# Kernel tuning notes

Hardware: AMD Instinct MI355X
Metric: run time of the kernel (lower is better)

## Reference

```python
import jax, jax.numpy as jnp
import numpy as np

N = 50000      # nodes
E = 800000     # edges (avg degree 16)
DIN = 128
HID = 128
OUT = 10       # classes
G = 64         # graphs in batch


def setup_inputs() -> dict:
    key = jax.random.key(0)
    ks = jax.random.split(key, 10)
    x = jax.random.normal(ks[0], (N, DIN), dtype=jnp.float32)
    edge_index = jax.random.randint(ks[1], (2, E), 0, N, dtype=jnp.int32)
    edge_weight = jax.random.uniform(ks[2], (E,), dtype=jnp.float32)
    batch = jnp.sort(jax.random.randint(ks[3], (N,), 0, G, dtype=jnp.int32))
    W1 = jax.random.normal(ks[4], (DIN, HID), dtype=jnp.float32) / np.sqrt(DIN)
    b1 = jnp.zeros((HID,), dtype=jnp.float32)
    W2 = jax.random.normal(ks[5], (HID, HID), dtype=jnp.float32) / np.sqrt(HID)
    b2 = jnp.zeros((HID,), dtype=jnp.float32)
    W3 = jax.random.normal(ks[6], (HID, OUT), dtype=jnp.float32) / np.sqrt(HID)
    b3 = jnp.zeros((OUT,), dtype=jnp.float32)
    return {"x": x, "edge_index": edge_index, "edge_weight": edge_weight,
            "batch": batch, "W1": W1, "b1": b1, "W2": W2, "b2": b2,
            "W3": W3, "b3": b3}


def _gcn_norm(edge_index, edge_weight, n_nodes):
    # PyG gcn_norm: add self-loops with weight 1, D^-1/2 (A+I) D^-1/2
    loop = jnp.arange(n_nodes, dtype=edge_index.dtype)
    src = jnp.concatenate([edge_index[0], loop])
    dst = jnp.concatenate([edge_index[1], loop])
    w = jnp.concatenate([edge_weight, jnp.ones((n_nodes,), edge_weight.dtype)])
    deg = jax.ops.segment_sum(w, dst, num_segments=n_nodes)
    dinv = jnp.where(deg > 0, jax.lax.rsqrt(deg), 0.0)
    norm = dinv[src] * w * dinv[dst]
    return src, dst, norm


def _gcn_conv(x, W, b, src, dst, norm, n_nodes):
    h = x @ W                                      # [N, F] dense transform
    msg = norm[:, None] * h[src]                   # gather + scale  [E+N, F]
    out = jax.ops.segment_sum(msg, dst, num_segments=n_nodes)  # scatter-add
    return out + b


def reference(x, edge_index, edge_weight, batch, W1, b1, W2, b2, W3, b3):
    src, dst, norm = _gcn_norm(edge_index, edge_weight, N)
    h = jax.nn.relu(_gcn_conv(x, W1, b1, src, dst, norm, N))
    h = jax.nn.relu(_gcn_conv(h, W2, b2, src, dst, norm, N))
    h = _gcn_conv(h, W3, b3, src, dst, norm, N)    # [N, OUT]
    # global_mean_pool over graph ids
    sums = jax.ops.segment_sum(h, batch, num_segments=G)          # [G, OUT]
    cnts = jax.ops.segment_sum(jnp.ones((N,), h.dtype), batch, num_segments=G)
    pooled = sums / jnp.maximum(cnts, 1.0)[:, None]
    return jax.nn.log_softmax(pooled, axis=1)
```

## Files before the change

### kernel.cpp

```cpp
#include <hip/hip_runtime.h>
#include <math.h>

#define NN 50000
#define EE 800000
#define GG 64
#define FD 128
#define OUTD 10
#define NB 49

typedef __attribute__((ext_vector_type(8))) short s8v;
typedef __attribute__((ext_vector_type(4))) float f4v;

static __device__ inline unsigned short f2b(float f) {
    unsigned int u = __float_as_uint(f);
    return (unsigned short)((u + 0x7FFFu + ((u >> 16) & 1u)) >> 16);
}

#define DEG_SCALE 4294967296.0
#define DEG_MASK  ((1ull << 44) - 1)


__global__ void k_init(unsigned long long* packed, int n) {
    int i = blockIdx.x * blockDim.x + threadIdx.x;
    if (i < n) packed[i] = (1ull << 44) | (1ull << 32);
}

__global__ void k_degree(const int* __restrict__ dst, const float* __restrict__ w,
                         unsigned long long* packed, unsigned* __restrict__ rank, int e) {
    int i = blockIdx.x * blockDim.x + threadIdx.x;
    if (i >= e) return;
    unsigned long long q = (unsigned long long)((double)w[i] * DEG_SCALE + 0.5);
    unsigned long long old = atomicAdd(&packed[dst[i]], (1ull << 44) | q);
    rank[i] = (unsigned)(old >> 44) - 1u;
}

__global__ void k_dinv(const unsigned long long* __restrict__ packed,
                       int* __restrict__ cnt, float* __restrict__ dinv, int n) {
    int i = blockIdx.x * blockDim.x + threadIdx.x;
    if (i >= n) return;
    unsigned long long p = packed[i];
    cnt[i] = (int)(p >> 44);
    float deg = (float)((double)(p & DEG_MASK) * (1.0 / DEG_SCALE));
    dinv[i] = 1.0f / sqrtf(deg);
}

__global__ __launch_bounds__(1024) void k_scanA(const int* __restrict__ cnt,
        int* __restrict__ rowptr, int* __restrict__ blocksum, int n) {
    __shared__ int wtot[16];
    int tid = threadIdx.x;
    int i = blockIdx.x * 1024 + tid;
    int lane = tid & 63, wv = tid >> 6;
    int v = (i < n) ? cnt[i] : 0;
    int s = v;
    #pragma unroll
    for (int off = 1; off < 64; off <<= 1) {
        int u = __shfl_up(s, off, 64);
        if (lane >= off) s += u;
    }
    if (lane == 63) wtot[wv] = s;
    __syncthreads();
    int wpre = 0;
    for (int j = 0; j < wv; ++j) wpre += wtot[j];
    if (i < n) rowptr[i] = wpre + s - v;
    if (tid == 1023) blocksum[blockIdx.x] = wpre + s;
}

__global__ void k_scanB(int* blocksum, int* rowptr) {
    int l = threadIdx.x;
    int v = (l < NB) ? blocksum[l] : 0;
    int s = v;
    #pragma unroll
    for (int off = 1; off < 64; off <<= 1) {
        int u = __shfl_up(s, off, 64);
        if (l >= off) s += u;
    }
    if (l < NB) blocksum[l] = s - v;
    if (l == NB - 1) rowptr[NN] = s;
}

__global__ __launch_bounds__(1024) void k_scanC(int* __restrict__ rowptr,
        const int* __restrict__ blocksum, int n) {
    int i = blockIdx.x * 1024 + threadIdx.x;
    if (i >= n) return;
    rowptr[i] += blocksum[blockIdx.x];
}

__global__ void k_fill(const int* __restrict__ src, const int* __restrict__ dst,
                       const float* __restrict__ w, const float* __restrict__ dinv,
                       const int* __restrict__ rowptr, const unsigned* __restrict__ rank,
                       uint2* __restrict__ ent, int e) {
    int i = blockIdx.x * blockDim.x + threadIdx.x;
    if (i >= e) return;
    int s = src[i], d = dst[i];
    int pos = rowptr[d] + (int)rank[i];
    float v = dinv[s] * w[i] * dinv[d];
    ent[pos] = make_uint2((unsigned)s, __float_as_uint(v));
}

__global__ void k_selfloop(const int* __restrict__ rowptr, const float* __restrict__ dinv,
                           uint2* __restrict__ ent, int n) {
    int i = blockIdx.x * blockDim.x + threadIdx.x;
    if (i >= n) return;
    float di = dinv[i];
    ent[rowptr[i + 1] - 1] = make_uint2((unsigned)i, __float_as_uint(di * di));
}

__global__ void k_bounds(const int* __restrict__ batch, int* __restrict__ gstart, int n) {
    int i = blockIdx.x * blockDim.x + threadIdx.x;
    if (i >= n) return;
    int b = batch[i];
    int bp = (i == 0) ? -1 : batch[i - 1];
    for (int g = bp + 1; g <= b; ++g) gstart[g] = i;
    if (i == n - 1)
        for (int g = b + 1; g <= GG; ++g) gstart[g] = n;
}


__global__ void k_cvt(const float* __restrict__ in, unsigned short* __restrict__ out, int n8) {
    int i = blockIdx.x * blockDim.x + threadIdx.x;
    if (i >= n8) return;
    const float4* p = (const float4*)in + (size_t)i * 2;
    float4 a = p[0], b = p[1];
    uint4 r;
    r.x = (unsigned)f2b(a.x) | ((unsigned)f2b(a.y) << 16);
    r.y = (unsigned)f2b(a.z) | ((unsigned)f2b(a.w) << 16);
    r.z = (unsigned)f2b(b.x) | ((unsigned)f2b(b.y) << 16);
    r.w = (unsigned)f2b(b.z) | ((unsigned)f2b(b.w) << 16);
    *((uint4*)out + i) = r;
}

__global__ void k_w128t(const float* __restrict__ W, unsigned short* __restrict__ Wt) {
    int i = blockIdx.x * blockDim.x + threadIdx.x;
    if (i >= FD * FD) return;
    int nn = i >> 7, k = i & 127;
    Wt[i] = f2b(W[k * FD + nn]);
}

__global__ __launch_bounds__(256) void k_gemm_bf(const unsigned short* __restrict__ A,
        const unsigned short* __restrict__ Wt, unsigned short* __restrict__ out, int n) {
    int tid = threadIdx.x;
    int wave = tid >> 6, lane = tid & 63;
    int quad = lane >> 4, c16 = lane & 15;
    int rowbase = blockIdx.x * 64 + wave * 16;
    int rowA = rowbase + c16;
    if (rowA >= n) rowA = n - 1;
    f4v acc[8];
    #pragma unroll
    for (int t = 0; t < 8; ++t) acc[t] = (f4v){0.f, 0.f, 0.f, 0.f};

    #pragma unroll
    for (int k0 = 0; k0 < 128; k0 += 32) {
        s8v a = *(const s8v*)(A + (size_t)rowA * FD + k0 + quad * 8);
        #pragma unroll
        for (int t = 0; t < 8; ++t) {
            s8v b = *(const s8v*)(Wt + (size_t)(t * 16 + c16) * FD + k0 + quad * 8);
            acc[t] = __builtin_amdgcn_mfma_f32_16x16x32_bf16(a, b, acc[t], 0, 0, 0);
        }
    }
    #pragma unroll
    for (int t = 0; t < 8; ++t) {
        #pragma unroll
        for (int r = 0; r < 4; ++r) {
            int row = rowbase + quad * 4 + r;
            if (row < n) out[(size_t)row * FD + t * 16 + c16] = f2b(acc[t][r]);
        }
    }
}

__global__ void k_gemm10(const unsigned short* __restrict__ A, const float* __restrict__ W,
                         float* __restrict__ out, int n) {
    __shared__ float Ws[FD * OUTD];
    int tid = threadIdx.x;
    for (int i = tid; i < FD * OUTD; i += blockDim.x) Ws[i] = W[i];
    __syncthreads();
    int i = blockIdx.x * blockDim.x + tid;
    if (i >= n) return;
    float acc[OUTD];
    #pragma unroll
    for (int c = 0; c < OUTD; ++c) acc[c] = 0.0f;
    const unsigned short* a = A + (size_t)i * FD;
    for (int k0 = 0; k0 < FD; k0 += 8) {
        uint4 t = *(const uint4*)(a + k0);
        float av[8];
        av[0] = __uint_as_float(t.x << 16); av[1] = __uint_as_float(t.x & 0xFFFF0000u);
        av[2] = __uint_as_float(t.y << 16); av[3] = __uint_as_float(t.y & 0xFFFF0000u);
        av[4] = __uint_as_float(t.z << 16); av[5] = __uint_as_float(t.z & 0xFFFF0000u);
        av[6] = __uint_as_float(t.w << 16); av[7] = __uint_as_float(t.w & 0xFFFF0000u);
        #pragma unroll
        for (int j = 0; j < 8; ++j)
            #pragma unroll
            for (int c = 0; c < OUTD; ++c) acc[c] += av[j] * Ws[(k0 + j) * OUTD + c];
    }
    float* o = out + (size_t)i * OUTD;
    #pragma unroll
    for (int c = 0; c < OUTD; ++c) o[c] = acc[c];
}

__global__ __launch_bounds__(256) void k_spmm_bf(const int* __restrict__ rowptr,
        const uint2* __restrict__ ent, const unsigned short* __restrict__ tin,
        const float* __restrict__ bias, unsigned short* __restrict__ out,
        int n, int dorelu) {
    int w = (blockIdx.x * blockDim.x + threadIdx.x) >> 6;
    int lane = threadIdx.x & 63;
    if (w >= n) return;
    int c = lane & 15, g = lane >> 4;
    int beg = rowptr[w], end = rowptr[w + 1];
    float acc[8];
    #pragma unroll
    for (int j = 0; j < 8; ++j) acc[j] = 0.0f;
    for (int e0 = beg; e0 < end; e0 += 8) {
        int e1 = e0 + g, e2 = e0 + 4 + g;
        uint2 en1 = (e1 < end) ? ent[e1] : make_uint2(0u, 0u);
        uint2 en2 = (e2 < end) ? ent[e2] : make_uint2(0u, 0u);
        uint4 t1 = *(const uint4*)(tin + (size_t)en1.x * FD + c * 8);
        uint4 t2 = *(const uint4*)(tin + (size_t)en2.x * FD + c * 8);
        float v1 = __uint_as_float(en1.y), v2 = __uint_as_float(en2.y);
        acc[0] += v1 * __uint_as_float(t1.x << 16);
        acc[1] += v1 * __uint_as_float(t1.x & 0xFFFF0000u);
        acc[2] += v1 * __uint_as_float(t1.y << 16);
        acc[3] += v1 * __uint_as_float(t1.y & 0xFFFF0000u);
        acc[4] += v1 * __uint_as_float(t1.z << 16);
        acc[5] += v1 * __uint_as_float(t1.z & 0xFFFF0000u);
        acc[6] += v1 * __uint_as_float(t1.w << 16);
        acc[7] += v1 * __uint_as_float(t1.w & 0xFFFF0000u);
        acc[0] += v2 * __uint_as_float(t2.x << 16);
        acc[1] += v2 * __uint_as_float(t2.x & 0xFFFF0000u);
        acc[2] += v2 * __uint_as_float(t2.y << 16);
        acc[3] += v2 * __uint_as_float(t2.y & 0xFFFF0000u);
        acc[4] += v2 * __uint_as_float(t2.z << 16);
        acc[5] += v2 * __uint_as_float(t2.z & 0xFFFF0000u);
        acc[6] += v2 * __uint_as_float(t2.w << 16);
        acc[7] += v2 * __uint_as_float(t2.w & 0xFFFF0000u);
    }
    #pragma unroll
    for (int j = 0; j < 8; ++j) {
        acc[j] += __shfl_xor(acc[j], 16, 64);
        acc[j] += __shfl_xor(acc[j], 32, 64);
    }
    if (g == 0) {
        uint4 r;
        float o[8];
        #pragma unroll
        for (int j = 0; j < 8; ++j) {
            float x = acc[j] + bias[c * 8 + j];
            o[j] = dorelu ? fmaxf(x, 0.0f) : x;
        }
        r.x = (unsigned)f2b(o[0]) | ((unsigned)f2b(o[1]) << 16);
        r.y = (unsigned)f2b(o[2]) | ((unsigned)f2b(o[3]) << 16);
        r.z = (unsigned)f2b(o[4]) | ((unsigned)f2b(o[5]) << 16);
        r.w = (unsigned)f2b(o[6]) | ((unsigned)f2b(o[7]) << 16);
        *(uint4*)(out + (size_t)w * FD + c * 8) = r;
    }
}

__global__ void k_spmm10(const int* __restrict__ rowptr, const uint2* __restrict__ ent,
        const float* __restrict__ tin, const float* __restrict__ bias,
        float* __restrict__ out, int n) {
    int t = blockIdx.x * blockDim.x + threadIdx.x;
    int node = t / OUTD;
    int c = t - node * OUTD;
    if (node >= n) return;
    int beg = rowptr[node], end = rowptr[node + 1];
    float acc = 0.0f;
    for (int e = beg; e < end; ++e) {
        uint2 en = ent[e];
        acc += __uint_as_float(en.y) * tin[(size_t)en.x * OUTD + c];
    }
    out[(size_t)node * OUTD + c] = acc + bias[c];
}


__global__ __launch_bounds__(256) void k_poolfin(const float* __restrict__ h,
        const int* __restrict__ gstart, float* __restrict__ out) {
    int g = blockIdx.x;
    int beg = gstart[g], end = gstart[g + 1];
    int tid = threadIdx.x;
    int lane = tid & 63, wv = tid >> 6;
    float acc[OUTD];
    #pragma unroll
    for (int c = 0; c < OUTD; ++c) acc[c] = 0.0f;
    for (int i = beg + tid; i < end; i += 256) {
        const float* hp = h + (size_t)i * OUTD;
        #pragma unroll
        for (int c = 0; c < OUTD; ++c) acc[c] += hp[c];
    }
    #pragma unroll
    for (int off = 32; off >= 1; off >>= 1)
        #pragma unroll
        for (int c = 0; c < OUTD; ++c) acc[c] += __shfl_down(acc[c], off, 64);
    __shared__ float ws[4][OUTD];
    if (lane == 0)
        #pragma unroll
        for (int c = 0; c < OUTD; ++c) ws[wv][c] = acc[c];
    __syncthreads();
    if (tid == 0) {
        float cf = fmaxf((float)(end - beg), 1.0f);
        float v[OUTD], m = -1e30f;
        #pragma unroll
        for (int c = 0; c < OUTD; ++c) {
            v[c] = (ws[0][c] + ws[1][c] + ws[2][c] + ws[3][c]) / cf;
            m = fmaxf(m, v[c]);
        }
        float s = 0.0f;
        #pragma unroll
        for (int c = 0; c < OUTD; ++c) s += expf(v[c] - m);
        float l = logf(s);
        #pragma unroll
        for (int c = 0; c < OUTD; ++c) out[g * OUTD + c] = v[c] - m - l;
    }
}


extern "C" void kernel_launch(void* const* d_in, const int* in_sizes, int n_in,
                              void* d_out, int out_size, void* d_ws, size_t ws_size,
                              hipStream_t stream) {
    const float* x   = (const float*)d_in[0];
    const int*   ei  = (const int*)d_in[1];
    const float* ew  = (const float*)d_in[2];
    const int*   bat = (const int*)d_in[3];
    const float* W1  = (const float*)d_in[4];
    const float* b1  = (const float*)d_in[5];
    const float* W2  = (const float*)d_in[6];
    const float* b2  = (const float*)d_in[7];
    const float* W3  = (const float*)d_in[8];
    const float* b3  = (const float*)d_in[9];
    float* out = (float*)d_out;

    const int* src = ei;
    const int* dst = ei + EE;

    char* p = (char*)d_ws;
    auto alloc = [&](size_t bytes) -> void* {
        void* r = (void*)p;
        p += (bytes + 255) & ~(size_t)255;
        return r;
    };
    unsigned long long* packed = (unsigned long long*)alloc((size_t)NN * 8);
    int*            cnt    = (int*)  alloc((size_t)NN * 4);
    float*          dinv   = (float*)alloc((size_t)NN * 4);
    int*            rowptr = (int*)  alloc((size_t)(NN + 1) * 4);
    unsigned*       rank   = (unsigned*)alloc((size_t)EE * 4);
    uint2*          ent    = (uint2*)alloc((size_t)(EE + NN) * 8);
    unsigned short* xbf    = (unsigned short*)alloc((size_t)NN * FD * 2);
    unsigned short* Wt1    = (unsigned short*)alloc((size_t)FD * FD * 2);
    unsigned short* Wt2    = (unsigned short*)alloc((size_t)FD * FD * 2);
    unsigned short* hA     = (unsigned short*)alloc((size_t)NN * FD * 2);
    unsigned short* hB     = (unsigned short*)alloc((size_t)NN * FD * 2);
    float*          bufC   = (float*)alloc((size_t)NN * OUTD * 4);
    float*          bufD   = (float*)alloc((size_t)NN * OUTD * 4);
    int*            bsum   = (int*)  alloc((size_t)(NB + 1) * 4);
    int*            gstart = (int*)  alloc((size_t)(GG + 1) * 4);
    (void)ws_size; (void)in_sizes; (void)n_in; (void)out_size;

    const int B = 256;
    k_init    <<<(NN + B - 1) / B, B, 0, stream>>>(packed, NN);
    k_degree  <<<(EE + B - 1) / B, B, 0, stream>>>(dst, ew, packed, rank, EE);
    k_dinv    <<<(NN + B - 1) / B, B, 0, stream>>>(packed, cnt, dinv, NN);
    k_scanA   <<<NB, 1024, 0, stream>>>(cnt, rowptr, bsum, NN);
    k_scanB   <<<1, 64, 0, stream>>>(bsum, rowptr);
    k_scanC   <<<NB, 1024, 0, stream>>>(rowptr, bsum, NN);
    k_fill    <<<(EE + B - 1) / B, B, 0, stream>>>(src, dst, ew, dinv, rowptr, rank, ent, EE);
    k_selfloop<<<(NN + B - 1) / B, B, 0, stream>>>(rowptr, dinv, ent, NN);
    k_bounds  <<<(NN + B - 1) / B, B, 0, stream>>>(bat, gstart, NN);
    k_cvt     <<<(NN * FD / 8 + B - 1) / B, B, 0, stream>>>(x, xbf, NN * FD / 8);
    k_w128t   <<<(FD * FD + B - 1) / B, B, 0, stream>>>(W1, Wt1);
    k_w128t   <<<(FD * FD + B - 1) / B, B, 0, stream>>>(W2, Wt2);

    k_gemm_bf<<<(NN + 63) / 64, B, 0, stream>>>(xbf, Wt1, hA, NN);
    k_spmm_bf<<<(NN * 64 + B - 1) / B, B, 0, stream>>>(rowptr, ent, hA, b1, hB, NN, 1);
    k_gemm_bf<<<(NN + 63) / 64, B, 0, stream>>>(hB, Wt2, hA, NN);
    k_spmm_bf<<<(NN * 64 + B - 1) / B, B, 0, stream>>>(rowptr, ent, hA, b2, hB, NN, 1);
    k_gemm10 <<<(NN + B - 1) / B, B, 0, stream>>>(hB, W3, bufC, NN);
    k_spmm10 <<<(NN * OUTD + B - 1) / B, B, 0, stream>>>(rowptr, ent, bufC, b3, bufD, NN);
    k_poolfin<<<GG, 256, 0, stream>>>(bufD, gstart, out);
}
```

Before: 309.2 us.

## Fuse preprocessing kernels, convert input in GEMM, deepen SpMM edge unrolling

Merges the weight transposes into the init kernel, the dinv computation into the first scan pass, and the self-loop insertion into the final scan pass, cutting several kernel launches and intermediate buffers. The first GEMM now reads fp32 x directly and rounds it to bf16 in registers, so the separate conversion pass and its extra round trip through memory go away. The SpMM inner loop now handles 16 edges per iteration with four independent gathers in flight, raising memory-level parallelism at the cost of more registers.

```diff
diff --git a/kernel.cpp b/kernel.cpp
--- a/kernel.cpp
+++ b/kernel.cpp
@@ -20,9 +20,16 @@
 #define DEG_MASK  ((1ull << 44) - 1)
 
 
-__global__ void k_init(unsigned long long* packed, int n) {
+__global__ void k_prep(unsigned long long* packed, const float* __restrict__ W1,
+                       const float* __restrict__ W2, unsigned short* __restrict__ Wt1,
+                       unsigned short* __restrict__ Wt2, int n) {
     int i = blockIdx.x * blockDim.x + threadIdx.x;
     if (i < n) packed[i] = (1ull << 44) | (1ull << 32);
+    if (i < FD * FD) {
+        int nn = i >> 7, k = i & 127;
+        Wt1[i] = f2b(W1[k * FD + nn]);
+        Wt2[i] = f2b(W2[k * FD + nn]);
+    }
 }
 
 __global__ void k_degree(const int* __restrict__ dst, const float* __restrict__ w,
@@ -34,23 +41,20 @@
     rank[i] = (unsigned)(old >> 44) - 1u;
 }
 
-__global__ void k_dinv(const unsigned long long* __restrict__ packed,
-                       int* __restrict__ cnt, float* __restrict__ dinv, int n) {
-    int i = blockIdx.x * blockDim.x + threadIdx.x;
-    if (i >= n) return;
-    unsigned long long p = packed[i];
-    cnt[i] = (int)(p >> 44);
-    float deg = (float)((double)(p & DEG_MASK) * (1.0 / DEG_SCALE));
-    dinv[i] = 1.0f / sqrtf(deg);
-}
-
-__global__ __launch_bounds__(1024) void k_scanA(const int* __restrict__ cnt,
-        int* __restrict__ rowptr, int* __restrict__ blocksum, int n) {
+__global__ __launch_bounds__(1024) void k_scanA(const unsigned long long* __restrict__ packed,
+        int* __restrict__ rowptr, int* __restrict__ blocksum,
+        float* __restrict__ dinv, int n) {
     __shared__ int wtot[16];
     int tid = threadIdx.x;
     int i = blockIdx.x * 1024 + tid;
     int lane = tid & 63, wv = tid >> 6;
-    int v = (i < n) ? cnt[i] : 0;
+    int v = 0;
+    if (i < n) {
+        unsigned long long p = packed[i];
+        v = (int)(p >> 44);
+        float deg = (float)((double)(p & DEG_MASK) * (1.0 / DEG_SCALE));
+        dinv[i] = 1.0f / sqrtf(deg);
+    }
     int s = v;
     #pragma unroll
     for (int off = 1; off < 64; off <<= 1) {
@@ -79,10 +83,15 @@
 }
 
 __global__ __launch_bounds__(1024) void k_scanC(int* __restrict__ rowptr,
-        const int* __restrict__ blocksum, int n) {
+        const int* __restrict__ blocksum, const unsigned long long* __restrict__ packed,
+        const float* __restrict__ dinv, uint2* __restrict__ ent, int n) {
     int i = blockIdx.x * 1024 + threadIdx.x;
     if (i >= n) return;
-    rowptr[i] += blocksum[blockIdx.x];
+    int r = rowptr[i] + blocksum[blockIdx.x];
+    rowptr[i] = r;
+    int cnt = (int)(packed[i] >> 44);
+    float di = dinv[i];
+    ent[r + cnt - 1] = make_uint2((unsigned)i, __float_as_uint(di * di));
 }
 
 __global__ void k_fill(const int* __restrict__ src, const int* __restrict__ dst,
@@ -97,14 +106,6 @@
     ent[pos] = make_uint2((unsigned)s, __float_as_uint(v));
 }
 
-__global__ void k_selfloop(const int* __restrict__ rowptr, const float* __restrict__ dinv,
-                           uint2* __restrict__ ent, int n) {
-    int i = blockIdx.x * blockDim.x + threadIdx.x;
-    if (i >= n) return;
-    float di = dinv[i];
-    ent[rowptr[i + 1] - 1] = make_uint2((unsigned)i, __float_as_uint(di * di));
-}
-
 __global__ void k_bounds(const int* __restrict__ batch, int* __restrict__ gstart, int n) {
     int i = blockIdx.x * blockDim.x + threadIdx.x;
     if (i >= n) return;
@@ -115,25 +116,42 @@
         for (int g = b + 1; g <= GG; ++g) gstart[g] = n;
 }
 
-
-__global__ void k_cvt(const float* __restrict__ in, unsigned short* __restrict__ out, int n8) {
-    int i = blockIdx.x * blockDim.x + threadIdx.x;
-    if (i >= n8) return;
-    const float4* p = (const float4*)in + (size_t)i * 2;
-    float4 a = p[0], b = p[1];
-    uint4 r;
-    r.x = (unsigned)f2b(a.x) | ((unsigned)f2b(a.y) << 16);
-    r.y = (unsigned)f2b(a.z) | ((unsigned)f2b(a.w) << 16);
-    r.z = (unsigned)f2b(b.x) | ((unsigned)f2b(b.y) << 16);
-    r.w = (unsigned)f2b(b.z) | ((unsigned)f2b(b.w) << 16);
-    *((uint4*)out + i) = r;
-}
-
-__global__ void k_w128t(const float* __restrict__ W, unsigned short* __restrict__ Wt) {
-    int i = blockIdx.x * blockDim.x + threadIdx.x;
-    if (i >= FD * FD) return;
-    int nn = i >> 7, k = i & 127;
-    Wt[i] = f2b(W[k * FD + nn]);
+__global__ __launch_bounds__(256) void k_gemm_f32in(const float* __restrict__ A,
+        const unsigned short* __restrict__ Wt, unsigned short* __restrict__ out, int n) {
+    int tid = threadIdx.x;
+    int wave = tid >> 6, lane = tid & 63;
+    int quad = lane >> 4, c16 = lane & 15;
+    int rowbase = blockIdx.x * 64 + wave * 16;
+    int rowA = rowbase + c16;
+    if (rowA >= n) rowA = n - 1;
+    f4v acc[8];
+    #pragma unroll
+    for (int t = 0; t < 8; ++t) acc[t] = (f4v){0.f, 0.f, 0.f, 0.f};
+
+    #pragma unroll
+    for (int k0 = 0; k0 < 128; k0 += 32) {
+        const float* ap = A + (size_t)rowA * FD + k0 + quad * 8;
+        float4 a0 = *(const float4*)ap;
+        float4 a1 = *(const float4*)(ap + 4);
+        s8v a;
+        a[0] = (short)f2b(a0.x); a[1] = (short)f2b(a0.y);
+        a[2] = (short)f2b(a0.z); a[3] = (short)f2b(a0.w);
+        a[4] = (short)f2b(a1.x); a[5] = (short)f2b(a1.y);
+        a[6] = (short)f2b(a1.z); a[7] = (short)f2b(a1.w);
+        #pragma unroll
+        for (int t = 0; t < 8; ++t) {
+            s8v b = *(const s8v*)(Wt + (size_t)(t * 16 + c16) * FD + k0 + quad * 8);
+            acc[t] = __builtin_amdgcn_mfma_f32_16x16x32_bf16(a, b, acc[t], 0, 0, 0);
+        }
+    }
+    #pragma unroll
+    for (int t = 0; t < 8; ++t) {
+        #pragma unroll
+        for (int r = 0; r < 4; ++r) {
+            int row = rowbase + quad * 4 + r;
+            if (row < n) out[(size_t)row * FD + t * 16 + c16] = f2b(acc[t][r]);
+        }
+    }
 }
 
 __global__ __launch_bounds__(256) void k_gemm_bf(const unsigned short* __restrict__ A,
@@ -208,29 +226,29 @@
     float acc[8];
     #pragma unroll
     for (int j = 0; j < 8; ++j) acc[j] = 0.0f;
-    for (int e0 = beg; e0 < end; e0 += 8) {
-        int e1 = e0 + g, e2 = e0 + 4 + g;
-        uint2 en1 = (e1 < end) ? ent[e1] : make_uint2(0u, 0u);
-        uint2 en2 = (e2 < end) ? ent[e2] : make_uint2(0u, 0u);
-        uint4 t1 = *(const uint4*)(tin + (size_t)en1.x * FD + c * 8);
-        uint4 t2 = *(const uint4*)(tin + (size_t)en2.x * FD + c * 8);
-        float v1 = __uint_as_float(en1.y), v2 = __uint_as_float(en2.y);
-        acc[0] += v1 * __uint_as_float(t1.x << 16);
-        acc[1] += v1 * __uint_as_float(t1.x & 0xFFFF0000u);
-        acc[2] += v1 * __uint_as_float(t1.y << 16);
-        acc[3] += v1 * __uint_as_float(t1.y & 0xFFFF0000u);
-        acc[4] += v1 * __uint_as_float(t1.z << 16);
-        acc[5] += v1 * __uint_as_float(t1.z & 0xFFFF0000u);
-        acc[6] += v1 * __uint_as_float(t1.w << 16);
-        acc[7] += v1 * __uint_as_float(t1.w & 0xFFFF0000u);
-        acc[0] += v2 * __uint_as_float(t2.x << 16);
-        acc[1] += v2 * __uint_as_float(t2.x & 0xFFFF0000u);
-        acc[2] += v2 * __uint_as_float(t2.y << 16);
-        acc[3] += v2 * __uint_as_float(t2.y & 0xFFFF0000u);
-        acc[4] += v2 * __uint_as_float(t2.z << 16);
-        acc[5] += v2 * __uint_as_float(t2.z & 0xFFFF0000u);
-        acc[6] += v2 * __uint_as_float(t2.w << 16);
-        acc[7] += v2 * __uint_as_float(t2.w & 0xFFFF0000u);
+    for (int e0 = beg; e0 < end; e0 += 16) {
+        uint2 en[4];
+        uint4 t[4];
+        #pragma unroll
+        for (int u = 0; u < 4; ++u) {
+            int e = e0 + 4 * u + g;
+            en[u] = (e < end) ? ent[e] : make_uint2(0u, 0u);
+        }
+        #pragma unroll
+        for (int u = 0; u < 4; ++u)
+            t[u] = *(const uint4*)(tin + (size_t)en[u].x * FD + c * 8);
+        #pragma unroll
+        for (int u = 0; u < 4; ++u) {
+            float v = __uint_as_float(en[u].y);
+            acc[0] += v * __uint_as_float(t[u].x << 16);
+            acc[1] += v * __uint_as_float(t[u].x & 0xFFFF0000u);
+            acc[2] += v * __uint_as_float(t[u].y << 16);
+            acc[3] += v * __uint_as_float(t[u].y & 0xFFFF0000u);
+            acc[4] += v * __uint_as_float(t[u].z << 16);
+            acc[5] += v * __uint_as_float(t[u].z & 0xFFFF0000u);
+            acc[6] += v * __uint_as_float(t[u].w << 16);
+            acc[7] += v * __uint_as_float(t[u].w & 0xFFFF0000u);
+        }
     }
     #pragma unroll
     for (int j = 0; j < 8; ++j) {
@@ -336,12 +354,10 @@
         return r;
     };
     unsigned long long* packed = (unsigned long long*)alloc((size_t)NN * 8);
-    int*            cnt    = (int*)  alloc((size_t)NN * 4);
     float*          dinv   = (float*)alloc((size_t)NN * 4);
     int*            rowptr = (int*)  alloc((size_t)(NN + 1) * 4);
     unsigned*       rank   = (unsigned*)alloc((size_t)EE * 4);
     uint2*          ent    = (uint2*)alloc((size_t)(EE + NN) * 8);
-    unsigned short* xbf    = (unsigned short*)alloc((size_t)NN * FD * 2);
     unsigned short* Wt1    = (unsigned short*)alloc((size_t)FD * FD * 2);
     unsigned short* Wt2    = (unsigned short*)alloc((size_t)FD * FD * 2);
     unsigned short* hA     = (unsigned short*)alloc((size_t)NN * FD * 2);
@@ -353,24 +369,19 @@
     (void)ws_size; (void)in_sizes; (void)n_in; (void)out_size;
 
     const int B = 256;
-    k_init    <<<(NN + B - 1) / B, B, 0, stream>>>(packed, NN);
-    k_degree  <<<(EE + B - 1) / B, B, 0, stream>>>(dst, ew, packed, rank, EE);
-    k_dinv    <<<(NN + B - 1) / B, B, 0, stream>>>(packed, cnt, dinv, NN);
-    k_scanA   <<<NB, 1024, 0, stream>>>(cnt, rowptr, bsum, NN);
-    k_scanB   <<<1, 64, 0, stream>>>(bsum, rowptr);
-    k_scanC   <<<NB, 1024, 0, stream>>>(rowptr, bsum, NN);
-    k_fill    <<<(EE + B - 1) / B, B, 0, stream>>>(src, dst, ew, dinv, rowptr, rank, ent, EE);
-    k_selfloop<<<(NN + B - 1) / B, B, 0, stream>>>(rowptr, dinv, ent, NN);
-    k_bounds  <<<(NN + B - 1) / B, B, 0, stream>>>(bat, gstart, NN);
-    k_cvt     <<<(NN * FD / 8 + B - 1) / B, B, 0, stream>>>(x, xbf, NN * FD / 8);
-    k_w128t   <<<(FD * FD + B - 1) / B, B, 0, stream>>>(W1, Wt1);
-    k_w128t   <<<(FD * FD + B - 1) / B, B, 0, stream>>>(W2, Wt2);
-
-    k_gemm_bf<<<(NN + 63) / 64, B, 0, stream>>>(xbf, Wt1, hA, NN);
-    k_spmm_bf<<<(NN * 64 + B - 1) / B, B, 0, stream>>>(rowptr, ent, hA, b1, hB, NN, 1);
-    k_gemm_bf<<<(NN + 63) / 64, B, 0, stream>>>(hB, Wt2, hA, NN);
-    k_spmm_bf<<<(NN * 64 + B - 1) / B, B, 0, stream>>>(rowptr, ent, hA, b2, hB, NN, 1);
-    k_gemm10 <<<(NN + B - 1) / B, B, 0, stream>>>(hB, W3, bufC, NN);
-    k_spmm10 <<<(NN * OUTD + B - 1) / B, B, 0, stream>>>(rowptr, ent, bufC, b3, bufD, NN);
-    k_poolfin<<<GG, 256, 0, stream>>>(bufD, gstart, out);
-}
+    k_prep  <<<(NN + B - 1) / B, B, 0, stream>>>(packed, W1, W2, Wt1, Wt2, NN);
+    k_degree<<<(EE + B - 1) / B, B, 0, stream>>>(dst, ew, packed, rank, EE);
+    k_scanA <<<NB, 1024, 0, stream>>>(packed, rowptr, bsum, dinv, NN);
+    k_scanB <<<1, 64, 0, stream>>>(bsum, rowptr);
+    k_scanC <<<NB, 1024, 0, stream>>>(rowptr, bsum, packed, dinv, ent, NN);
+    k_fill  <<<(EE + B - 1) / B, B, 0, stream>>>(src, dst, ew, dinv, rowptr, rank, ent, EE);
+    k_bounds<<<(NN + B - 1) / B, B, 0, stream>>>(bat, gstart, NN);
+
+    k_gemm_f32in<<<(NN + 63) / 64, B, 0, stream>>>(x, Wt1, hA, NN);
+    k_spmm_bf   <<<(NN * 64 + B - 1) / B, B, 0, stream>>>(rowptr, ent, hA, b1, hB, NN, 1);
+    k_gemm_bf   <<<(NN + 63) / 64, B, 0, stream>>>(hB, Wt2, hA, NN);
+    k_spmm_bf   <<<(NN * 64 + B - 1) / B, B, 0, stream>>>(rowptr, ent, hA, b2, hB, NN, 1);
+    k_gemm10    <<<(NN + B - 1) / B, B, 0, stream>>>(hB, W3, bufC, NN);
+    k_spmm10    <<<(NN * OUTD + B - 1) / B, B, 0, stream>>>(rowptr, ent, bufC, b3, bufD, NN);
+    k_poolfin   <<<GG, 256, 0, stream>>>(bufD, gstart, out);
+}
```

New measurement: 297.3 us. 1.04x faster.
